# Optimization experiments

Measured on AMD Instinct MI355X. Metric: run time of the kernel, lower is better.

## Reference

```python
import jax, jax.numpy as jnp
import numpy as np

OUTPUT_BIT = 8
N_SCALE = 28          # scale_bits
EXP_BITS = 16
SEGMENTS = 16
DEGREE = 2
S_VAL = 0.03          # input quantization scale


def _fit_pieces(s):
    # Mirrors _compute_integer_coefficients for backend='float':
    # fit exp((x_off-127)*s) over offset domain x_off*s in [-128s, 127s].
    xs_off = np.linspace(-128.0, 127.0, 10000)
    ys = np.exp((xs_off - 127.0) * s)
    xs = xs_off * s
    bounds = np.linspace(-128.0 * s, 127.0 * s, SEGMENTS + 1)
    coeffs = np.zeros((SEGMENTS, DEGREE + 1))  # ascending powers a0,a1,a2
    for j in range(SEGMENTS):
        m = (xs >= bounds[j]) & (xs <= bounds[j + 1])
        coeffs[j] = np.polyfit(xs[m], ys[m], DEGREE)[::-1]
    # integer coefficients: p(x_int*s)*2^N = sum_k floor(a_k*s^k*2^N)*x_int^k
    pw = s ** np.arange(DEGREE + 1)
    coeffs_int = np.floor(coeffs * pw[None, :] * (2.0 ** N_SCALE))
    lo_int = np.floor(bounds[:-1] / s)  # integer segment lower bounds
    return lo_int.astype(np.float32), coeffs_int.astype(np.float32)


def setup_inputs() -> dict:
    key = jax.random.key(0)
    x = jax.random.normal(key, (8, 12, 512, 512), dtype=jnp.float32) * 4.0
    scaling_factor = jnp.full((1,), S_VAL, dtype=jnp.float32)
    lo_np, cf_np = _fit_pieces(S_VAL)
    return {
        "x": x,
        "scaling_factor": scaling_factor,
        "lo_bounds": jnp.asarray(lo_np),
        "coeffs": jnp.asarray(cf_np),
    }


def floor_ste(y):
    # floor with straight-through gradient
    return y + jax.lax.stop_gradient(jnp.floor(y) - y)


def reference(x, scaling_factor, lo_bounds, coeffs):
    s = scaling_factor
    x_int = floor_ste(x / s)
    x_int = x_int - jnp.max(x_int, axis=-1, keepdims=True) + 127.0

    # piecewise-polynomial integer exp (computed under no_grad in the original)
    xi = jax.lax.stop_gradient(x_int)
    idx = jnp.clip(jnp.searchsorted(lo_bounds, xi, side="right") - 1, 0, SEGMENTS - 1)
    c = coeffs[idx]                         # [..., deg+1], ascending powers
    r = c[..., DEGREE]
    for k in range(DEGREE - 1, -1, -1):     # Horner evaluation
        r = r * xi + c[..., k]
    exp_int = jnp.maximum(jax.lax.stop_gradient(r), 0.0)

    exp_int = floor_ste(exp_int / 2.0 ** (30 - EXP_BITS + 1))
    exp_sum = jnp.maximum(jnp.sum(exp_int, axis=-1, keepdims=True), 1.0)
    factor = jnp.floor(2.0 ** 32 / jax.lax.stop_gradient(exp_sum))
    softmax_int = jnp.floor(jax.lax.stop_gradient(exp_int) * factor / 2.0 ** (32 - OUTPUT_BIT + 1))

    softmax_float = jax.nn.softmax(x, axis=-1)
    s_out = jnp.array([2.0 / 2 ** OUTPUT_BIT], dtype=x.dtype)
    smi_f = softmax_int * s_out
    # STE: integer value forward, float-softmax gradient backward
    output = jax.lax.stop_gradient(smi_f) + (softmax_float - jax.lax.stop_gradient(softmax_float))
    output = s_out * floor_ste(output / s_out)
    return output, s_out
```

## Files before the change

### kernel.cpp

```cpp
#include <hip/hip_runtime.h>


#define ROWLEN 512

__global__ __launch_bounds__(256) void ppis_kernel(
    const float* __restrict__ x,
    const float* __restrict__ sfp,
    const float* __restrict__ lo,
    const float* __restrict__ cf,
    float* __restrict__ out,
    int nrows)
{
    __shared__ int4 s_cf[16];

    const int tid  = threadIdx.x;
    const int lane = tid & 63;
    const int wid  = tid >> 6;

    if (tid < 16)
        s_cf[tid] = make_int4((int)cf[tid*3+0], (int)cf[tid*3+1], (int)cf[tid*3+2], 0);

    const double sd = (double)sfp[0];
    const double y  = 1.0 / sd;
    __syncthreads();

    const long long row = (long long)blockIdx.x * 4 + wid;
    const float4* xp = reinterpret_cast<const float4*>(x) + row * (ROWLEN / 4);
    const float4 v0 = xp[lane];
    const float4 v1 = xp[lane + 64];

    const float xv[8] = {v0.x, v0.y, v0.z, v0.w, v1.x, v1.y, v1.z, v1.w};

    int n[8];
    #pragma unroll
    for (int k = 0; k < 8; ++k) {
        const double xd = (double)xv[k];
        const double q0 = xd * y;
        const double rr = fma(-sd, q0, xd);
        const double q  = fma(rr, y, q0);
        n[k] = (int)floor(q);
    }

    int mx = n[0];
    #pragma unroll
    for (int k = 1; k < 8; ++k) mx = max(mx, n[k]);
    #pragma unroll
    for (int off = 32; off >= 1; off >>= 1)
        mx = max(mx, __shfl_xor(mx, off, 64));

    const int off255 = 255 - mx;

    int e[8];
    int tsum = 0;
    #pragma unroll
    for (int k = 0; k < 8; ++k) {
        const int u  = n[k] + off255;
        const int uc = u < 0 ? 0 : u;
        int idx = ((uc + 1) * 257) >> 12;
        idx = idx > 15 ? 15 : idx;
        const int4 c = s_cf[idx];
        const int xi = u - 128;
        const int r1 = c.z * xi + c.y;
        long long r2 = (long long)r1 * xi + c.x;
        if (r2 < 0) r2 = 0;
        e[k] = (int)(r2 >> 15);
        tsum += e[k];
    }

    #pragma unroll
    for (int off = 32; off >= 1; off >>= 1)
        tsum += __shfl_xor(tsum, off, 64);
    if (tsum < 1) tsum = 1;

    const double factor = floor(__ddiv_rn(4294967296.0, (double)tsum));

    float o[8];
    #pragma unroll
    for (int k = 0; k < 8; ++k) {
        const int si = (int)((double)e[k] * factor * 2.9802322387695312e-08);
        o[k] = (float)si * 0.0078125f;
    }

    float4* op = reinterpret_cast<float4*>(out) + row * (ROWLEN / 4);
    op[lane]      = make_float4(o[0], o[1], o[2], o[3]);
    op[lane + 64] = make_float4(o[4], o[5], o[6], o[7]);

    if (row == 0 && tid == 0)
        out[(long long)nrows * ROWLEN] = 0.0078125f;
}

extern "C" void kernel_launch(void* const* d_in, const int* in_sizes, int n_in,
                              void* d_out, int out_size, void* d_ws, size_t ws_size,
                              hipStream_t stream) {
    const float* x  = (const float*)d_in[0];
    const float* sf = (const float*)d_in[1];
    const float* lo = (const float*)d_in[2];
    const float* cf = (const float*)d_in[3];
    float* out = (float*)d_out;

    const int nrows = in_sizes[0] / ROWLEN;
    ppis_kernel<<<nrows / 4, 256, 0, stream>>>(x, sf, lo, cf, out, nrows);
}
```

Measured before the change: 182.5 us.

## Process one row per half-wave, integer rescale, nontemporal stores

Each 32-lane half-wave now handles a full row with four float4 loads per lane, so a block covers eight rows and the reductions use 32-wide shuffles. The final double-precision multiply and scale is replaced with a 64-bit integer multiply and shift. Output is written with nontemporal stores to avoid polluting the cache. More loads in flight per thread should improve memory-level parallelism for this bandwidth-bound kernel, at the cost of more registers and half as many blocks.

```diff
diff --git a/kernel.cpp b/kernel.cpp
--- a/kernel.cpp
+++ b/kernel.cpp
@@ -2,6 +2,8 @@
 
 
 #define ROWLEN 512
+
+typedef float nfloat4 __attribute__((ext_vector_type(4)));
 
 __global__ __launch_bounds__(256) void ppis_kernel(
     const float* __restrict__ x,
@@ -16,6 +18,8 @@
     const int tid  = threadIdx.x;
     const int lane = tid & 63;
     const int wid  = tid >> 6;
+    const int half = lane >> 5;
+    const int hl   = lane & 31;
 
     if (tid < 16)
         s_cf[tid] = make_int4((int)cf[tid*3+0], (int)cf[tid*3+1], (int)cf[tid*3+2], 0);
@@ -24,17 +28,18 @@
     const double y  = 1.0 / sd;
     __syncthreads();
 
-    const long long row = (long long)blockIdx.x * 4 + wid;
-    const float4* xp = reinterpret_cast<const float4*>(x) + row * (ROWLEN / 4);
-    const float4 v0 = xp[lane];
-    const float4 v1 = xp[lane + 64];
+    const long long row = (long long)blockIdx.x * 8 + wid * 2 + half;
+    const float4* xp = reinterpret_cast<const float4*>(x) + row * (ROWLEN / 4) + hl;
 
-    const float xv[8] = {v0.x, v0.y, v0.z, v0.w, v1.x, v1.y, v1.z, v1.w};
+    float4 v[4];
+    #pragma unroll
+    for (int j = 0; j < 4; ++j) v[j] = xp[j * 32];
 
-    int n[8];
+    int n[16];
+    const float* vf = reinterpret_cast<const float*>(v);
     #pragma unroll
-    for (int k = 0; k < 8; ++k) {
-        const double xd = (double)xv[k];
+    for (int k = 0; k < 16; ++k) {
+        const double xd = (double)vf[k];
         const double q0 = xd * y;
         const double rr = fma(-sd, q0, xd);
         const double q  = fma(rr, y, q0);
@@ -43,17 +48,17 @@
 
     int mx = n[0];
     #pragma unroll
-    for (int k = 1; k < 8; ++k) mx = max(mx, n[k]);
+    for (int k = 1; k < 16; ++k) mx = max(mx, n[k]);
     #pragma unroll
-    for (int off = 32; off >= 1; off >>= 1)
-        mx = max(mx, __shfl_xor(mx, off, 64));
+    for (int off = 16; off >= 1; off >>= 1)
+        mx = max(mx, __shfl_xor(mx, off, 32));
 
     const int off255 = 255 - mx;
 
-    int e[8];
+    int e[16];
     int tsum = 0;
     #pragma unroll
-    for (int k = 0; k < 8; ++k) {
+    for (int k = 0; k < 16; ++k) {
         const int u  = n[k] + off255;
         const int uc = u < 0 ? 0 : u;
         int idx = ((uc + 1) * 257) >> 12;
@@ -68,24 +73,28 @@
     }
 
     #pragma unroll
-    for (int off = 32; off >= 1; off >>= 1)
-        tsum += __shfl_xor(tsum, off, 64);
+    for (int off = 16; off >= 1; off >>= 1)
+        tsum += __shfl_xor(tsum, off, 32);
     if (tsum < 1) tsum = 1;
 
-    const double factor = floor(__ddiv_rn(4294967296.0, (double)tsum));
+    const unsigned int factor =
+        (unsigned int)floor(__ddiv_rn(4294967296.0, (double)tsum));
 
-    float o[8];
+    nfloat4 o[4];
+    float* of = reinterpret_cast<float*>(o);
     #pragma unroll
-    for (int k = 0; k < 8; ++k) {
-        const int si = (int)((double)e[k] * factor * 2.9802322387695312e-08);
-        o[k] = (float)si * 0.0078125f;
+    for (int k = 0; k < 16; ++k) {
+        const unsigned long long p = (unsigned long long)(unsigned int)e[k] * factor;
+        const int si = (int)(p >> 25);
+        of[k] = (float)si * 0.0078125f;
     }
 
-    float4* op = reinterpret_cast<float4*>(out) + row * (ROWLEN / 4);
-    op[lane]      = make_float4(o[0], o[1], o[2], o[3]);
-    op[lane + 64] = make_float4(o[4], o[5], o[6], o[7]);
+    nfloat4* op = reinterpret_cast<nfloat4*>(out) + row * (ROWLEN / 4) + hl;
+    #pragma unroll
+    for (int j = 0; j < 4; ++j)
+        __builtin_nontemporal_store(o[j], &op[j * 32]);
 
-    if (row == 0 && tid == 0)
+    if (row == 0 && lane == 0)
         out[(long long)nrows * ROWLEN] = 0.0078125f;
 }
 
@@ -99,5 +108,5 @@
     float* out = (float*)d_out;
 
     const int nrows = in_sizes[0] / ROWLEN;
-    ppis_kernel<<<nrows / 4, 256, 0, stream>>>(x, sf, lo, cf, out, nrows);
+    ppis_kernel<<<nrows / 8, 256, 0, stream>>>(x, sf, lo, cf, out, nrows);
 }
```

Result: no change. 181.9 us (-0.3%).

## Process six rows per wave with prefetch, fp32 floor-division, integer scaling, nontemporal stores

Applied to the files above, without the earlier changes.

Each wave now handles six consecutive rows and prefetches the next row's data while computing the current one, which overlaps load latency and amortizes block setup. The double-precision division used for quantization is replaced by an fp32 floor with exact correction steps. The final scaling becomes a 64-bit integer multiply and shift instead of double math. Outputs are written with nontemporal stores. The row count must be divisible by 24 (49152 rows is), and the fp32 correction has to match the double-precision floor exactly.

```diff
diff --git a/kernel.cpp b/kernel.cpp
--- a/kernel.cpp
+++ b/kernel.cpp
@@ -2,8 +2,11 @@
 
 
 #define ROWLEN 512
+#define ROWS_PER_WAVE 6
 
-__global__ __launch_bounds__(256) void ppis_kernel(
+typedef float nfloat4 __attribute__((ext_vector_type(4)));
+
+__global__ __launch_bounds__(256, 8) void ppis_kernel(
     const float* __restrict__ x,
     const float* __restrict__ sfp,
     const float* __restrict__ lo,
@@ -20,72 +23,95 @@
     if (tid < 16)
         s_cf[tid] = make_int4((int)cf[tid*3+0], (int)cf[tid*3+1], (int)cf[tid*3+2], 0);
 
-    const double sd = (double)sfp[0];
-    const double y  = 1.0 / sd;
+    const float s  = sfp[0];
+    const float ry = 1.0f / s;
     __syncthreads();
 
-    const long long row = (long long)blockIdx.x * 4 + wid;
-    const float4* xp = reinterpret_cast<const float4*>(x) + row * (ROWLEN / 4);
-    const float4 v0 = xp[lane];
-    const float4 v1 = xp[lane + 64];
+    const long long wgid = (long long)blockIdx.x * 4 + wid;
+    const long long row0 = wgid * ROWS_PER_WAVE;
 
-    const float xv[8] = {v0.x, v0.y, v0.z, v0.w, v1.x, v1.y, v1.z, v1.w};
+    const float4* xbase = reinterpret_cast<const float4*>(x);
+    nfloat4*      obase = reinterpret_cast<nfloat4*>(out);
 
-    int n[8];
-    #pragma unroll
-    for (int k = 0; k < 8; ++k) {
-        const double xd = (double)xv[k];
-        const double q0 = xd * y;
-        const double rr = fma(-sd, q0, xd);
-        const double q  = fma(rr, y, q0);
-        n[k] = (int)floor(q);
-    }
-
-    int mx = n[0];
-    #pragma unroll
-    for (int k = 1; k < 8; ++k) mx = max(mx, n[k]);
-    #pragma unroll
-    for (int off = 32; off >= 1; off >>= 1)
-        mx = max(mx, __shfl_xor(mx, off, 64));
-
-    const int off255 = 255 - mx;
-
-    int e[8];
-    int tsum = 0;
-    #pragma unroll
-    for (int k = 0; k < 8; ++k) {
-        const int u  = n[k] + off255;
-        const int uc = u < 0 ? 0 : u;
-        int idx = ((uc + 1) * 257) >> 12;
-        idx = idx > 15 ? 15 : idx;
-        const int4 c = s_cf[idx];
-        const int xi = u - 128;
-        const int r1 = c.z * xi + c.y;
-        long long r2 = (long long)r1 * xi + c.x;
-        if (r2 < 0) r2 = 0;
-        e[k] = (int)(r2 >> 15);
-        tsum += e[k];
+    float4 na, nb;
+    {
+        const float4* xp = xbase + row0 * (ROWLEN / 4);
+        na = xp[lane];
+        nb = xp[lane + 64];
     }
 
     #pragma unroll
-    for (int off = 32; off >= 1; off >>= 1)
-        tsum += __shfl_xor(tsum, off, 64);
-    if (tsum < 1) tsum = 1;
+    for (int r = 0; r < ROWS_PER_WAVE; ++r) {
+        const long long row = row0 + r;
+        const float4 va = na, vb = nb;
+        if (r + 1 < ROWS_PER_WAVE) {
+            const float4* xp = xbase + (row + 1) * (ROWLEN / 4);
+            na = xp[lane];
+            nb = xp[lane + 64];
+        }
 
-    const double factor = floor(__ddiv_rn(4294967296.0, (double)tsum));
+        const float xv[8] = {va.x, va.y, va.z, va.w, vb.x, vb.y, vb.z, vb.w};
 
-    float o[8];
-    #pragma unroll
-    for (int k = 0; k < 8; ++k) {
-        const int si = (int)((double)e[k] * factor * 2.9802322387695312e-08);
-        o[k] = (float)si * 0.0078125f;
+        int n[8];
+        #pragma unroll
+        for (int k = 0; k < 8; ++k) {
+            const float xk = xv[k];
+            float nf = floorf(xk * ry);
+            const float d = fmaf(-s, nf, xk);
+            nf = (d < 0.0f) ? nf - 1.0f : nf;
+            const float u = fmaf(-s, nf + 1.0f, xk);
+            nf = (u >= 0.0f) ? nf + 1.0f : nf;
+            n[k] = (int)nf;
+        }
+
+        int mx = max(max(max(n[0], n[1]), max(n[2], n[3])),
+                     max(max(n[4], n[5]), max(n[6], n[7])));
+        #pragma unroll
+        for (int off = 32; off >= 1; off >>= 1)
+            mx = max(mx, __shfl_xor(mx, off, 64));
+
+        const int off255 = 255 - mx;
+
+        int e[8];
+        int tsum = 0;
+        #pragma unroll
+        for (int k = 0; k < 8; ++k) {
+            const int u  = n[k] + off255;
+            const int uc = u < 0 ? 0 : u;
+            int idx = ((uc + 1) * 257) >> 12;
+            idx = idx > 15 ? 15 : idx;
+            const int4 c = s_cf[idx];
+            const int xi = u - 128;
+            const int r1 = c.z * xi + c.y;
+            long long r2 = (long long)r1 * xi + c.x;
+            if (r2 < 0) r2 = 0;
+            e[k] = (int)(r2 >> 15);
+            tsum += e[k];
+        }
+
+        #pragma unroll
+        for (int off = 32; off >= 1; off >>= 1)
+            tsum += __shfl_xor(tsum, off, 64);
+        if (tsum < 1) tsum = 1;
+
+        const unsigned int factor =
+            (unsigned int)floor(__ddiv_rn(4294967296.0, (double)tsum));
+
+        nfloat4 o0, o1;
+        #pragma unroll
+        for (int k = 0; k < 4; ++k) {
+            const unsigned long long p0 = (unsigned long long)(unsigned int)e[k] * factor;
+            const unsigned long long p1 = (unsigned long long)(unsigned int)e[k+4] * factor;
+            o0[k] = (float)(int)(p0 >> 25) * 0.0078125f;
+            o1[k] = (float)(int)(p1 >> 25) * 0.0078125f;
+        }
+
+        nfloat4* op = obase + row * (ROWLEN / 4);
+        __builtin_nontemporal_store(o0, op + lane);
+        __builtin_nontemporal_store(o1, op + lane + 64);
     }
 
-    float4* op = reinterpret_cast<float4*>(out) + row * (ROWLEN / 4);
-    op[lane]      = make_float4(o[0], o[1], o[2], o[3]);
-    op[lane + 64] = make_float4(o[4], o[5], o[6], o[7]);
-
-    if (row == 0 && tid == 0)
+    if (wgid == 0 && lane == 0)
         out[(long long)nrows * ROWLEN] = 0.0078125f;
 }
 
@@ -99,5 +125,6 @@
     float* out = (float*)d_out;
 
     const int nrows = in_sizes[0] / ROWLEN;
-    ppis_kernel<<<nrows / 4, 256, 0, stream>>>(x, sf, lo, cf, out, nrows);
+    const int blocks = nrows / (ROWS_PER_WAVE * 4);
+    ppis_kernel<<<blocks, 256, 0, stream>>>(x, sf, lo, cf, out, nrows);
 }
```

After: 190.9 us. 1.05x slower.
